# Optimization experiments

Measured on AMD Instinct MI355X. Metric: run time of the kernel, lower is better.

The kernel has to match this reference:

```python
import jax, jax.numpy as jnp
import numpy as np

NUM_CLUSTERS = 16
HIDDEN = 1024
BOTTLENECK = 128
N_TOKENS = 65536


def setup_inputs() -> dict:
    key = jax.random.key(0)
    k_h, k_ids, k_w1, k_b1, k_w2, k_b2 = jax.random.split(key, 6)
    h = jax.random.normal(k_h, (N_TOKENS, HIDDEN), dtype=jnp.float32)
    cluster_ids = jax.random.randint(k_ids, (N_TOKENS,), 0, NUM_CLUSTERS)
    # Stacked per-cluster adapter params (torch Linear: y = x @ W.T + b; we store
    # already-transposed weights so forward is x @ W1[c]).
    s1 = 1.0 / np.sqrt(HIDDEN)
    s2 = 1.0 / np.sqrt(BOTTLENECK)
    W1 = jax.random.uniform(k_w1, (NUM_CLUSTERS, HIDDEN, BOTTLENECK), jnp.float32, -s1, s1)
    b1 = jax.random.uniform(k_b1, (NUM_CLUSTERS, BOTTLENECK), jnp.float32, -s1, s1)
    # Original inits these to zero; use small random values so grads are non-trivial.
    W2 = jax.random.uniform(k_w2, (NUM_CLUSTERS, BOTTLENECK, HIDDEN), jnp.float32, -s2, s2) * 0.02
    b2 = jax.random.uniform(k_b2, (NUM_CLUSTERS, HIDDEN), jnp.float32, -s2, s2) * 0.02
    return {"h": h, "cluster_ids": cluster_ids, "W1": W1, "b1": b1, "W2": W2, "b2": b2}


def reference(h, cluster_ids, W1, b1, W2, b2):
    # h: [N, H]; cluster_ids: [N]; W1: [K, H, B]; b1: [K, B]; W2: [K, B, H]; b2: [K, H]
    # out[n] = h[n] + adapter_{cluster_ids[n]}(h[n])
    K = W1.shape[0]
    out = jnp.zeros_like(h)
    for c in range(K):  # fixed small expert count; select per-token result via where
        mid = jax.nn.gelu(h @ W1[c] + b1[c], approximate=False)  # [N, B]
        y = h + mid @ W2[c] + b2[c]                               # [N, H]
        out = jnp.where((cluster_ids == c)[:, None], y, out)
    return out
```

## Files before the change

### kernel.cpp

```cpp
#include <hip/hip_runtime.h>
#include <hip/hip_bf16.h>
#include <math.h>

#define NUM_CLUSTERS 16
#define HIDDEN 1024
#define BOT 128
#define NTOK 65536

typedef __attribute__((ext_vector_type(8))) short bf16x8;
typedef __attribute__((ext_vector_type(4))) float f32x4;

typedef __attribute__((address_space(3))) unsigned int lds_u32;
typedef const __attribute__((address_space(1))) unsigned int glb_u32;

__device__ __forceinline__ void gload16(const void* g, void* l) {
  __builtin_amdgcn_global_load_lds((glb_u32*)g, (lds_u32*)l, 16, 0, 0);
}

__device__ __forceinline__ unsigned short f2bf(float x) {
  union { float f; unsigned u; } v; v.f = x;
  unsigned r = v.u + 0x7fffu + ((v.u >> 16) & 1u);
  return (unsigned short)(r >> 16);
}

__device__ __forceinline__ bf16x8 pack8(float4 a, float4 b) {
  bf16x8 r;
  r[0] = (short)f2bf(a.x); r[1] = (short)f2bf(a.y);
  r[2] = (short)f2bf(a.z); r[3] = (short)f2bf(a.w);
  r[4] = (short)f2bf(b.x); r[5] = (short)f2bf(b.y);
  r[6] = (short)f2bf(b.z); r[7] = (short)f2bf(b.w);
  return r;
}

#define SWZS(row, sidx) ((sidx) ^ (((row) & 7) << 3))
#define SW4(row, fidx) ((fidx) ^ (((row) & 7) << 2))

#define SCB() __builtin_amdgcn_sched_barrier(0)
#define VMW(n)                                          \
  do {                                                  \
    SCB();                                              \
    asm volatile("s_waitcnt vmcnt(" #n ")" ::: "memory"); \
    SCB();                                              \
  } while (0)
#define SBAR()                                  \
  do {                                          \
    SCB();                                      \
    __builtin_amdgcn_s_barrier();               \
    SCB();                                      \
  } while (0)
#define LGKM0() asm volatile("s_waitcnt lgkmcnt(0)" ::: "memory")

__device__ __forceinline__ int xcd_swz(int bid, int nwg) {
  const int nx = 8;
  int q = nwg / nx, r = nwg % nx;
  int xcd = bid % nx, idx = bid / nx;
  int b = (xcd < r) ? xcd * (q + 1) : r * (q + 1) + (xcd - r) * q;
  return b + idx;
}


__global__ void k_zero(int* p) {
  if (threadIdx.x < 64) p[threadIdx.x] = 0;
}

__global__ void k_hist(const int* __restrict__ ids, int* __restrict__ counts) {
  __shared__ int lh[NUM_CLUSTERS];
  if (threadIdx.x < NUM_CLUSTERS) lh[threadIdx.x] = 0;
  __syncthreads();
  int i = blockIdx.x * blockDim.x + threadIdx.x;
  int stride = gridDim.x * blockDim.x;
  for (; i < NTOK; i += stride) atomicAdd(&lh[ids[i]], 1);
  __syncthreads();
  if (threadIdx.x < NUM_CLUSTERS) atomicAdd(&counts[threadIdx.x], lh[threadIdx.x]);
}

__global__ void k_scan(const int* __restrict__ counts, int* __restrict__ offsets,
                       int* __restrict__ cursor) {
  if (threadIdx.x == 0 && blockIdx.x == 0) {
    int s = 0;
    for (int c = 0; c < NUM_CLUSTERS; ++c) {
      offsets[c] = s; cursor[c] = s; s += counts[c];
    }
    offsets[NUM_CLUSTERS] = s;
  }
}

__global__ void k_scatter(const int* __restrict__ ids, int* cursor,
                          int* __restrict__ perm) {
  __shared__ int lh[NUM_CLUSTERS], lbase[NUM_CLUSTERS];
  const int tid = threadIdx.x;
  if (tid < NUM_CLUSTERS) lh[tid] = 0;
  __syncthreads();
  const int i = blockIdx.x * 256 + tid;
  const int cc = ids[i];
  const int r = atomicAdd(&lh[cc], 1);
  __syncthreads();
  if (tid < NUM_CLUSTERS) lbase[tid] = atomicAdd(&cursor[tid], lh[tid]);
  __syncthreads();
  perm[lbase[cc] + r] = i;
}

__global__ void k_w1til(const float* __restrict__ W1, unsigned short* __restrict__ outw) {
  const int id = blockIdx.x * 256 + threadIdx.x;
  const int c  = id >> 14;
  const int ks = (id >> 10) & 15;
  const int q  = id & 1023;
  const int o  = q << 4;
  const int row = o >> 7;
  const int lb  = (o & 127) ^ ((row & 7) << 4);
  const int k0  = ks * 64 + (lb >> 1);
  const float* src = W1 + ((size_t)c * HIDDEN + k0) * BOT + row;
  unsigned short v[8];
  #pragma unroll
  for (int j = 0; j < 8; ++j) v[j] = f2bf(src[(size_t)j * BOT]);
  *(uint4*)((char*)outw + ((size_t)(c * 16 + ks)) * 16384 + o) = *(const uint4*)v;
}

__global__ void k_w2til(const float* __restrict__ W2, unsigned short* __restrict__ outw) {
  const int id = blockIdx.x * 256 + threadIdx.x;
  const int c  = id >> 14;
  const int nc = (id >> 10) & 15;
  const int q  = id & 1023;
  const int o  = q << 4;
  const int row = o >> 8;
  const int lb  = (o & 255) ^ ((row & 7) << 4);
  const int b0  = lb >> 1;
  const int n   = nc * 64 + row;
  const float* src = W2 + ((size_t)c * BOT + b0) * HIDDEN + n;
  unsigned short v[8];
  #pragma unroll
  for (int j = 0; j < 8; ++j) v[j] = f2bf(src[(size_t)j * HIDDEN]);
  *(uint4*)((char*)outw + ((size_t)(c * 16 + nc)) * 16384 + o) = *(const uint4*)v;
}

__device__ __forceinline__ bool locate(const int* offsets, int bid, int TMv,
                                       int& c, int& base, int& nvalid) {
  int t = bid;
  for (c = 0; c < NUM_CLUSTERS; ++c) {
    int cnt = offsets[c + 1] - offsets[c];
    int nt = (cnt + TMv - 1) / TMv;
    if (t < nt) {
      base = offsets[c] + t * TMv;
      nvalid = min(TMv, offsets[c + 1] - base);
      return true;
    }
    t -= nt;
  }
  return false;
}


__global__ __launch_bounds__(512, 6) void k_gemm1(
    const float* __restrict__ h, const float* __restrict__ b1g,
    const unsigned short* __restrict__ W1til, const int* __restrict__ offsets,
    const int* __restrict__ perm, unsigned short* __restrict__ midg) {

  __shared__ __align__(16) unsigned short sA[2][4096];
  __shared__ __align__(16) unsigned short sB[2][8192];
  __shared__ int sTok[64];

  const int tid = threadIdx.x;
  const int l = tid & 63, w = tid >> 6;
  const int lr = l & 15, lg = l >> 4;
  const int wr = w >> 2, wc = w & 3;
  const int row = tid >> 3, o8 = tid & 7;

  const int nwg = NTOK / 64 + NUM_CLUSTERS;
  int c, base, nvalid;
  if (!locate(offsets, xcd_swz(blockIdx.x, nwg), 64, c, base, nvalid)) return;

  if (tid < 64) sTok[tid] = perm[base + min(tid, nvalid - 1)];
  LGKM0();
  SBAR();

  const unsigned short* w1base = W1til + (size_t)c * 16 * 8192;
  const float* hrow = h + (long)sTok[row] * HIDDEN + o8 * 8;

  float4 vaA[2], vaB[2];
  vaA[0] = *(const float4*)(hrow);       vaA[1] = *(const float4*)(hrow + 4);
  SCB();
  gload16(w1base + tid * 8, &sB[0][tid * 8]);
  gload16(w1base + 4096 + tid * 8, &sB[0][4096 + tid * 8]);
  SCB();
  vaB[0] = *(const float4*)(hrow + 64);  vaB[1] = *(const float4*)(hrow + 68);
  SCB();
  *(bf16x8*)&sA[0][SWZS(row, row * 64 + o8 * 8)] = pack8(vaA[0], vaA[1]);
  LGKM0();
  VMW(2);
  SBAR();

  f32x4 acc[2][2];
  #pragma unroll
  for (int i = 0; i < 2; ++i)
    #pragma unroll
    for (int j = 0; j < 2; ++j) { f32x4 z = {0.f, 0.f, 0.f, 0.f}; acc[i][j] = z; }

#define G1_MFMA(CUR)                                                          \
  do {                                                                        \
    _Pragma("unroll")                                                         \
    for (int kk = 0; kk < 2; ++kk) {                                          \
      bf16x8 af[2], bfr[2];                                                   \
      _Pragma("unroll")                                                       \
      for (int mf = 0; mf < 2; ++mf) {                                        \
        const int m = wr * 32 + mf * 16 + lr;                                 \
        af[mf] = *(const bf16x8*)&sA[CUR][SWZS(m, m * 64 + kk * 32 + lg * 8)];\
      }                                                                       \
      _Pragma("unroll")                                                       \
      for (int nf = 0; nf < 2; ++nf) {                                        \
        const int rn = wc * 32 + nf * 16 + lr;                                \
        bfr[nf] = *(const bf16x8*)&sB[CUR][SWZS(rn, rn * 64 + kk * 32 + lg * 8)]; \
      }                                                                       \
      _Pragma("unroll")                                                       \
      for (int mf = 0; mf < 2; ++mf)                                          \
        _Pragma("unroll")                                                     \
        for (int nf = 0; nf < 2; ++nf)                                        \
          acc[mf][nf] = __builtin_amdgcn_mfma_f32_16x16x32_bf16(              \
              af[mf], bfr[nf], acc[mf][nf], 0, 0, 0);                         \
    }                                                                         \
  } while (0)

  #pragma unroll
  for (int t = 0; t < 16; ++t) {
    const int cur = t & 1;
    if (t < 15) {
      const unsigned short* w1s = w1base + (t + 1) * 8192;
      gload16(w1s + tid * 8, &sB[cur ^ 1][tid * 8]);
      gload16(w1s + 4096 + tid * 8, &sB[cur ^ 1][4096 + tid * 8]);
      SCB();
    }
    if (t < 14) {
      if (t & 1) {
        vaB[0] = *(const float4*)(hrow + (t + 2) * 64);
        vaB[1] = *(const float4*)(hrow + (t + 2) * 64 + 4);
      } else {
        vaA[0] = *(const float4*)(hrow + (t + 2) * 64);
        vaA[1] = *(const float4*)(hrow + (t + 2) * 64 + 4);
      }
      SCB();
    }
    G1_MFMA(cur);
    if (t < 15) {
      const float4* src = ((t + 1) & 1) ? vaB : vaA;
      *(bf16x8*)&sA[cur ^ 1][SWZS(row, row * 64 + o8 * 8)] = pack8(src[0], src[1]);
      if (t < 14) { VMW(2); } else { VMW(0); }
      LGKM0();
      SBAR();
    }
  }
#undef G1_MFMA

  float b1v[2];
  #pragma unroll
  for (int nf = 0; nf < 2; ++nf) b1v[nf] = b1g[c * BOT + wc * 32 + nf * 16 + lr];
  #pragma unroll
  for (int mf = 0; mf < 2; ++mf) {
    #pragma unroll
    for (int nf = 0; nf < 2; ++nf) {
      #pragma unroll
      for (int r = 0; r < 4; ++r) {
        float x = acc[mf][nf][r] + b1v[nf];
        float g = 0.5f * x * (1.0f + erff(x * 0.70710678118654752f));
        const int m = wr * 32 + mf * 16 + lg * 4 + r;
        if (m < nvalid) {
          const int n = wc * 32 + nf * 16 + lr;
          midg[(size_t)(base + m) * BOT + n] = f2bf(g);
        }
      }
    }
  }
}


__global__ __launch_bounds__(512, 6) void k_gemm2(
    const float* __restrict__ h, const float* __restrict__ b2g,
    const unsigned short* __restrict__ W2til, const int* __restrict__ offsets,
    const int* __restrict__ perm, const unsigned short* __restrict__ midg,
    float* __restrict__ out) {

  __shared__ __align__(16) unsigned short sM[8192];
  __shared__ __align__(16) unsigned short sB[2][8192];
  __shared__ int sTok[64];

  const int tid = threadIdx.x;
  const int l = tid & 63, w = tid >> 6;
  const int lr = l & 15, lg = l >> 4;
  const int wr = w >> 2, wc = w & 3;
  const int erow = tid >> 3, eo = tid & 7;

  const int nwg = NTOK / 64 + NUM_CLUSTERS;
  int c, base, nvalid;
  if (!locate(offsets, xcd_swz(blockIdx.x, nwg), 64, c, base, nvalid)) return;

  if (tid < 64) sTok[tid] = perm[base + min(tid, nvalid - 1)];

  const unsigned short* w2base = W2til + (size_t)c * 16 * 8192;

  {
    const int srow = base + min(erow, nvalid - 1);
    const uint4* ms = (const uint4*)(midg + (size_t)srow * BOT + eo * 16);
    uint4 m0 = ms[0], m1 = ms[1];
    SCB();
    gload16(w2base + tid * 8, &sB[0][tid * 8]);
    gload16(w2base + 4096 + tid * 8, &sB[0][4096 + tid * 8]);
    SCB();
    *(uint4*)&sM[SWZS(erow, erow * 128 + eo * 16)]     = m0;
    *(uint4*)&sM[SWZS(erow, erow * 128 + eo * 16 + 8)] = m1;
  }
  LGKM0();
  VMW(0);
  SBAR();

  const long etok = (long)sTok[erow] * HIDDEN;
  const float* hrow = h + etok;
  float* orow = out + etok;
  const bool evalid = erow < nvalid;

  for (int nc = 0; nc < 16; ++nc) {
    const int cur = nc & 1;
    float4 hv0 = *(const float4*)(hrow + nc * 64 + eo * 8);
    float4 hv1 = *(const float4*)(hrow + nc * 64 + eo * 8 + 4);
    float4 bv0 = *(const float4*)(b2g + c * HIDDEN + nc * 64 + eo * 8);
    float4 bv1 = *(const float4*)(b2g + c * HIDDEN + nc * 64 + eo * 8 + 4);
    SCB();
    if (nc < 15) {
      const unsigned short* w2s = w2base + (nc + 1) * 8192;
      gload16(w2s + tid * 8, &sB[cur ^ 1][tid * 8]);
      gload16(w2s + 4096 + tid * 8, &sB[cur ^ 1][4096 + tid * 8]);
      SCB();
    }

    f32x4 acc[2];
    { f32x4 z = {0.f, 0.f, 0.f, 0.f}; acc[0] = z; acc[1] = z; }
    #pragma unroll
    for (int kk = 0; kk < 4; ++kk) {
      bf16x8 af[2], bf1;
      #pragma unroll
      for (int mf = 0; mf < 2; ++mf) {
        const int m = wr * 32 + mf * 16 + lr;
        af[mf] = *(const bf16x8*)&sM[SWZS(m, m * 128 + kk * 32 + lg * 8)];
      }
      const int rn = wc * 16 + lr;
      bf1 = *(const bf16x8*)&sB[cur][SWZS(rn, rn * 128 + kk * 32 + lg * 8)];
      #pragma unroll
      for (int mf = 0; mf < 2; ++mf)
        acc[mf] = __builtin_amdgcn_mfma_f32_16x16x32_bf16(af[mf], bf1, acc[mf], 0, 0, 0);
    }
    SBAR();

    float* sOutF = (float*)&sB[cur][0];
    #pragma unroll
    for (int mf = 0; mf < 2; ++mf) {
      #pragma unroll
      for (int r = 0; r < 4; ++r) {
        const int m = wr * 32 + mf * 16 + lg * 4 + r;
        const int n = wc * 16 + lr;
        sOutF[SW4(m, m * 64 + n)] = acc[mf][r];
      }
    }
    LGKM0();
    SBAR();

    if (evalid) {
      const int fb = erow * 64 + eo * 8;
      const float4 y0 = *(const float4*)&sOutF[SW4(erow, fb)];
      const float4 y1 = *(const float4*)&sOutF[SW4(erow, fb + 4)];
      float4 o0, o1;
      o0.x = y0.x + hv0.x + bv0.x; o0.y = y0.y + hv0.y + bv0.y;
      o0.z = y0.z + hv0.z + bv0.z; o0.w = y0.w + hv0.w + bv0.w;
      o1.x = y1.x + hv1.x + bv1.x; o1.y = y1.y + hv1.y + bv1.y;
      o1.z = y1.z + hv1.z + bv1.z; o1.w = y1.w + hv1.w + bv1.w;
      *(float4*)(orow + nc * 64 + eo * 8)     = o0;
      *(float4*)(orow + nc * 64 + eo * 8 + 4) = o1;
    }
    if (nc < 15) {
      VMW(2);
      SBAR();
    }
  }
}

#define FSWZ(row, sidx) ((sidx) ^ (((row) & 7) << 3))

__global__ __launch_bounds__(256, 2) void k_fused(
    const float* __restrict__ h, const float* __restrict__ b1g,
    const float* __restrict__ b2g, const unsigned short* __restrict__ W1til,
    const unsigned short* __restrict__ W2til, const int* __restrict__ offsets,
    const int* __restrict__ perm, float* __restrict__ out) {

  __shared__ __align__(16) unsigned short sAB[16384];
  __shared__ __align__(16) unsigned short sMid[16384];
  __shared__ int sTok[128];

  const int tid = threadIdx.x;
  const int l = tid & 63, w = tid >> 6;
  const int wr = w >> 1, wc = w & 1;
  const int lr = l & 15, lg = l >> 4;

  int c, base, nvalid;
  if (!locate(offsets, blockIdx.x, 128, c, base, nvalid)) return;

  if (tid < 128) sTok[tid] = perm[base + min(tid, nvalid - 1)];
  __syncthreads();

  const unsigned short* w1base = W1til + (size_t)c * 16 * 8192;
  const unsigned short* w2base = W2til + (size_t)c * 16 * 8192;

  const int arow = tid >> 1, ahalf = tid & 1;
  const long htok = (long)sTok[arow] * HIDDEN;

  f32x4 acc[4][4];
  #pragma unroll
  for (int i = 0; i < 4; ++i)
    #pragma unroll
    for (int j = 0; j < 4; ++j) { f32x4 z = {0.f, 0.f, 0.f, 0.f}; acc[i][j] = z; }

  for (int ks = 0; ks < 16; ++ks) {
    __syncthreads();
    const unsigned short* w1s = w1base + ks * 8192;
    #pragma unroll
    for (int j = 0; j < 4; ++j)
      gload16(w1s + j * 2048 + tid * 8, &sAB[8192 + j * 2048 + tid * 8]);
    {
      const float* hp = h + htok + ks * 64 + ahalf * 32;
      float4 v0 = *(const float4*)(hp + 0),  v1 = *(const float4*)(hp + 4);
      float4 v2 = *(const float4*)(hp + 8),  v3 = *(const float4*)(hp + 12);
      float4 v4 = *(const float4*)(hp + 16), v5 = *(const float4*)(hp + 20);
      float4 v6 = *(const float4*)(hp + 24), v7 = *(const float4*)(hp + 28);
      const int sb = arow * 64 + ahalf * 32;
      *(bf16x8*)&sAB[FSWZ(arow, sb + 0)]  = pack8(v0, v1);
      *(bf16x8*)&sAB[FSWZ(arow, sb + 8)]  = pack8(v2, v3);
      *(bf16x8*)&sAB[FSWZ(arow, sb + 16)] = pack8(v4, v5);
      *(bf16x8*)&sAB[FSWZ(arow, sb + 24)] = pack8(v6, v7);
    }
    __syncthreads();
    #pragma unroll
    for (int kk = 0; kk < 2; ++kk) {
      bf16x8 af[4], bfr[4];
      #pragma unroll
      for (int mf = 0; mf < 4; ++mf) {
        const int rw = wr * 64 + mf * 16 + lr;
        af[mf] = *(const bf16x8*)&sAB[FSWZ(rw, rw * 64 + kk * 32 + lg * 8)];
      }
      #pragma unroll
      for (int nf = 0; nf < 4; ++nf) {
        const int rn = wc * 64 + nf * 16 + lr;
        bfr[nf] = *(const bf16x8*)&sAB[8192 + FSWZ(rn, rn * 64 + kk * 32 + lg * 8)];
      }
      #pragma unroll
      for (int mf = 0; mf < 4; ++mf)
        #pragma unroll
        for (int nf = 0; nf < 4; ++nf)
          acc[mf][nf] = __builtin_amdgcn_mfma_f32_16x16x32_bf16(af[mf], bfr[nf], acc[mf][nf], 0, 0, 0);
    }
  }

  float b1v[4];
  #pragma unroll
  for (int nf = 0; nf < 4; ++nf) b1v[nf] = b1g[c * BOT + wc * 64 + nf * 16 + lr];
  #pragma unroll
  for (int mf = 0; mf < 4; ++mf)
    #pragma unroll
    for (int nf = 0; nf < 4; ++nf)
      #pragma unroll
      for (int r = 0; r < 4; ++r) {
        float x = acc[mf][nf][r] + b1v[nf];
        float g = 0.5f * x * (1.0f + erff(x * 0.70710678118654752f));
        const int m = wr * 64 + mf * 16 + lg * 4 + r;
        const int n = wc * 64 + nf * 16 + lr;
        sMid[FSWZ(m, m * 128 + n)] = f2bf(g);
      }

  for (int nc = 0; nc < 16; ++nc) {
    __syncthreads();
    #pragma unroll
    for (int j = 0; j < 4; ++j)
      gload16(w2base + nc * 8192 + j * 2048 + tid * 8, &sAB[j * 2048 + tid * 8]);
    __syncthreads();

    f32x4 a2[4][2];
    #pragma unroll
    for (int i = 0; i < 4; ++i)
      #pragma unroll
      for (int j = 0; j < 2; ++j) { f32x4 z = {0.f, 0.f, 0.f, 0.f}; a2[i][j] = z; }

    #pragma unroll
    for (int kk = 0; kk < 4; ++kk) {
      bf16x8 af[4], bfr[2];
      #pragma unroll
      for (int mf = 0; mf < 4; ++mf) {
        const int m = wr * 64 + mf * 16 + lr;
        af[mf] = *(const bf16x8*)&sMid[FSWZ(m, m * 128 + kk * 32 + lg * 8)];
      }
      #pragma unroll
      for (int nf = 0; nf < 2; ++nf) {
        const int rn = wc * 32 + nf * 16 + lr;
        bfr[nf] = *(const bf16x8*)&sAB[FSWZ(rn, rn * 128 + kk * 32 + lg * 8)];
      }
      #pragma unroll
      for (int mf = 0; mf < 4; ++mf)
        #pragma unroll
        for (int nf = 0; nf < 2; ++nf)
          a2[mf][nf] = __builtin_amdgcn_mfma_f32_16x16x32_bf16(af[mf], bfr[nf], a2[mf][nf], 0, 0, 0);
    }

    #pragma unroll
    for (int nf = 0; nf < 2; ++nf) {
      const int nn = nc * 64 + wc * 32 + nf * 16 + lr;
      const float b2v = b2g[c * HIDDEN + nn];
      #pragma unroll
      for (int mf = 0; mf < 4; ++mf)
        #pragma unroll
        for (int r = 0; r < 4; ++r) {
          const int m = wr * 64 + mf * 16 + lg * 4 + r;
          if (m < nvalid) {
            const long tk = (long)sTok[m] * HIDDEN;
            out[tk + nn] = h[tk + nn] + a2[mf][nf][r] + b2v;
          }
        }
    }
  }
}

extern "C" void kernel_launch(void* const* d_in, const int* in_sizes, int n_in,
                              void* d_out, int out_size, void* d_ws, size_t ws_size,
                              hipStream_t stream) {
  const float* h   = (const float*)d_in[0];
  const int*   ids = (const int*)d_in[1];
  const float* W1  = (const float*)d_in[2];
  const float* b1  = (const float*)d_in[3];
  const float* W2  = (const float*)d_in[4];
  const float* b2  = (const float*)d_in[5];
  float* out = (float*)d_out;

  char* ws = (char*)d_ws;
  int* counts  = (int*)ws;
  int* cursor  = (int*)(ws + 64);
  int* offsets = (int*)(ws + 128);
  int* perm    = (int*)(ws + 256);
  unsigned short* W1til = (unsigned short*)(ws + 262400);
  unsigned short* W2til = W1til + (size_t)16 * 16 * 8192;
  unsigned short* midg  = W2til + (size_t)16 * 16 * 8192;
  const size_t need = 262400 + 2 * (size_t)16 * 16 * 8192 * 2 +
                      (size_t)NTOK * BOT * 2;

  k_zero<<<1, 64, 0, stream>>>(counts);
  k_hist<<<256, 256, 0, stream>>>(ids, counts);
  k_scan<<<1, 64, 0, stream>>>(counts, offsets, cursor);
  k_scatter<<<NTOK / 256, 256, 0, stream>>>(ids, cursor, perm);
  k_w1til<<<1024, 256, 0, stream>>>(W1, W1til);
  k_w2til<<<1024, 256, 0, stream>>>(W2, W2til);

  if (ws_size >= need) {
    const int nwg = NTOK / 64 + NUM_CLUSTERS;
    k_gemm1<<<nwg, 512, 0, stream>>>(h, b1, W1til, offsets, perm, midg);
    k_gemm2<<<nwg, 512, 0, stream>>>(h, b2, W2til, offsets, perm, midg, out);
  } else {
    k_fused<<<NTOK / 128 + NUM_CLUSTERS, 256, 0, stream>>>(
        h, b1, b2, W1til, W2til, offsets, perm, out);
  }
}
```

Before: 270.3 us.

## Rewrite gemm2 to read fragment-ordered W2 directly from global, dropping LDS staging

Adds a k_w2lin prepack that stores W2 in MFMA B-fragment order, so each lane loads its operand with one contiguous 16-byte global read. k_gemm2 drops to 256 threads: each wave owns 16 token rows and keeps its mid A-fragments in registers, and all W2 staging through LDS is removed along with the block-wide barriers. LDS is now used only for a per-wave epilogue transpose. The cost is that every wave rereads W2 tiles from global/L2 instead of sharing them through LDS, and the per-wave work per block is larger.

Result: slower. 330.4 us (+22.2%).

```diff
diff --git a/kernel.cpp b/kernel.cpp
--- a/kernel.cpp
+++ b/kernel.cpp
@@ -116,6 +116,22 @@
   *(uint4*)((char*)outw + ((size_t)(c * 16 + ks)) * 16384 + o) = *(const uint4*)v;
 }
 
+__global__ void k_w2lin(const float* __restrict__ W2, unsigned short* __restrict__ outw) {
+  const int id = blockIdx.x * 256 + threadIdx.x;
+  const int c   = id >> 14;
+  const int rem = id & 16383;
+  const int fg  = rem >> 6;
+  const int l   = rem & 63;
+  const int nc  = fg >> 4, kk = (fg >> 2) & 3, nf = fg & 3;
+  const int n   = nc * 64 + nf * 16 + (l & 15);
+  const int k0  = kk * 32 + (l >> 4) * 8;
+  const float* src = W2 + ((size_t)c * BOT + k0) * HIDDEN + n;
+  unsigned short v[8];
+  #pragma unroll
+  for (int j = 0; j < 8; ++j) v[j] = f2bf(src[(size_t)j * HIDDEN]);
+  *(uint4*)(outw + (size_t)id * 8) = *(const uint4*)v;
+}
+
 __global__ void k_w2til(const float* __restrict__ W2, unsigned short* __restrict__ outw) {
   const int id = blockIdx.x * 256 + threadIdx.x;
   const int c  = id >> 14;
@@ -148,7 +164,6 @@
   }
   return false;
 }
-
 
 __global__ __launch_bounds__(512, 6) void k_gemm1(
     const float* __restrict__ h, const float* __restrict__ b1g,
@@ -271,110 +286,87 @@
 }
 
 
-__global__ __launch_bounds__(512, 6) void k_gemm2(
+__global__ __launch_bounds__(256, 5) void k_gemm2(
     const float* __restrict__ h, const float* __restrict__ b2g,
-    const unsigned short* __restrict__ W2til, const int* __restrict__ offsets,
+    const unsigned short* __restrict__ W2lin, const int* __restrict__ offsets,
     const int* __restrict__ perm, const unsigned short* __restrict__ midg,
     float* __restrict__ out) {
 
-  __shared__ __align__(16) unsigned short sM[8192];
-  __shared__ __align__(16) unsigned short sB[2][8192];
+  __shared__ __align__(16) float sOut[4 * 1024];
   __shared__ int sTok[64];
 
   const int tid = threadIdx.x;
   const int l = tid & 63, w = tid >> 6;
   const int lr = l & 15, lg = l >> 4;
-  const int wr = w >> 2, wc = w & 3;
-  const int erow = tid >> 3, eo = tid & 7;
 
   const int nwg = NTOK / 64 + NUM_CLUSTERS;
   int c, base, nvalid;
   if (!locate(offsets, xcd_swz(blockIdx.x, nwg), 64, c, base, nvalid)) return;
 
   if (tid < 64) sTok[tid] = perm[base + min(tid, nvalid - 1)];
-
-  const unsigned short* w2base = W2til + (size_t)c * 16 * 8192;
-
-  {
-    const int srow = base + min(erow, nvalid - 1);
-    const uint4* ms = (const uint4*)(midg + (size_t)srow * BOT + eo * 16);
-    uint4 m0 = ms[0], m1 = ms[1];
-    SCB();
-    gload16(w2base + tid * 8, &sB[0][tid * 8]);
-    gload16(w2base + 4096 + tid * 8, &sB[0][4096 + tid * 8]);
-    SCB();
-    *(uint4*)&sM[SWZS(erow, erow * 128 + eo * 16)]     = m0;
-    *(uint4*)&sM[SWZS(erow, erow * 128 + eo * 16 + 8)] = m1;
-  }
-  LGKM0();
-  VMW(0);
-  SBAR();
-
+  __syncthreads();
+
+  const long amrow = (long)(base + min(w * 16 + lr, nvalid - 1)) * BOT;
+  bf16x8 ma[4];
+  #pragma unroll
+  for (int kk = 0; kk < 4; ++kk)
+    ma[kk] = *(const bf16x8*)(midg + amrow + kk * 32 + lg * 8);
+
+  const unsigned short* wlin = W2lin + (size_t)c * 131072;
+
+  const int er = l >> 2, ecg = l & 3;
+  const int erow = w * 16 + er;
+  const bool evalid = erow < nvalid;
   const long etok = (long)sTok[erow] * HIDDEN;
   const float* hrow = h + etok;
   float* orow = out + etok;
-  const bool evalid = erow < nvalid;
+  float* sW = sOut + w * 1024;
+  const float* b2c = b2g + c * HIDDEN;
 
   for (int nc = 0; nc < 16; ++nc) {
-    const int cur = nc & 1;
-    float4 hv0 = *(const float4*)(hrow + nc * 64 + eo * 8);
-    float4 hv1 = *(const float4*)(hrow + nc * 64 + eo * 8 + 4);
-    float4 bv0 = *(const float4*)(b2g + c * HIDDEN + nc * 64 + eo * 8);
-    float4 bv1 = *(const float4*)(b2g + c * HIDDEN + nc * 64 + eo * 8 + 4);
-    SCB();
-    if (nc < 15) {
-      const unsigned short* w2s = w2base + (nc + 1) * 8192;
-      gload16(w2s + tid * 8, &sB[cur ^ 1][tid * 8]);
-      gload16(w2s + 4096 + tid * 8, &sB[cur ^ 1][4096 + tid * 8]);
-      SCB();
-    }
-
-    f32x4 acc[2];
-    { f32x4 z = {0.f, 0.f, 0.f, 0.f}; acc[0] = z; acc[1] = z; }
+    const unsigned short* fbp = wlin + nc * 8192;
+
+    f32x4 acc[4];
+    #pragma unroll
+    for (int i = 0; i < 4; ++i) { f32x4 z = {0.f, 0.f, 0.f, 0.f}; acc[i] = z; }
+
     #pragma unroll
     for (int kk = 0; kk < 4; ++kk) {
-      bf16x8 af[2], bf1;
-      #pragma unroll
-      for (int mf = 0; mf < 2; ++mf) {
-        const int m = wr * 32 + mf * 16 + lr;
-        af[mf] = *(const bf16x8*)&sM[SWZS(m, m * 128 + kk * 32 + lg * 8)];
-      }
-      const int rn = wc * 16 + lr;
-      bf1 = *(const bf16x8*)&sB[cur][SWZS(rn, rn * 128 + kk * 32 + lg * 8)];
-      #pragma unroll
-      for (int mf = 0; mf < 2; ++mf)
-        acc[mf] = __builtin_amdgcn_mfma_f32_16x16x32_bf16(af[mf], bf1, acc[mf], 0, 0, 0);
-    }
-    SBAR();
-
-    float* sOutF = (float*)&sB[cur][0];
-    #pragma unroll
-    for (int mf = 0; mf < 2; ++mf) {
+      #pragma unroll
+      for (int nf = 0; nf < 4; ++nf) {
+        const bf16x8 bf = *(const bf16x8*)(fbp + (kk * 4 + nf) * 512 + l * 8);
+        acc[nf] = __builtin_amdgcn_mfma_f32_16x16x32_bf16(ma[kk], bf, acc[nf], 0, 0, 0);
+      }
+    }
+
+    float4 hv[4], bv[4];
+    #pragma unroll
+    for (int j = 0; j < 4; ++j) {
+      hv[j] = *(const float4*)(hrow + nc * 64 + ecg * 16 + j * 4);
+      bv[j] = *(const float4*)(b2c + nc * 64 + ecg * 16 + j * 4);
+    }
+
+    #pragma unroll
+    for (int nf = 0; nf < 4; ++nf) {
       #pragma unroll
       for (int r = 0; r < 4; ++r) {
-        const int m = wr * 32 + mf * 16 + lg * 4 + r;
-        const int n = wc * 16 + lr;
-        sOutF[SW4(m, m * 64 + n)] = acc[mf][r];
-      }
-    }
-    LGKM0();
-    SBAR();
-
+        const int m = lg * 4 + r;
+        const int n = nf * 16 + lr;
+        sW[SW4(m, m * 64 + n)] = acc[nf][r];
+      }
+    }
     if (evalid) {
-      const int fb = erow * 64 + eo * 8;
-      const float4 y0 = *(const float4*)&sOutF[SW4(erow, fb)];
-      const float4 y1 = *(const float4*)&sOutF[SW4(erow, fb + 4)];
-      float4 o0, o1;
-      o0.x = y0.x + hv0.x + bv0.x; o0.y = y0.y + hv0.y + bv0.y;
-      o0.z = y0.z + hv0.z + bv0.z; o0.w = y0.w + hv0.w + bv0.w;
-      o1.x = y1.x + hv1.x + bv1.x; o1.y = y1.y + hv1.y + bv1.y;
-      o1.z = y1.z + hv1.z + bv1.z; o1.w = y1.w + hv1.w + bv1.w;
-      *(float4*)(orow + nc * 64 + eo * 8)     = o0;
-      *(float4*)(orow + nc * 64 + eo * 8 + 4) = o1;
-    }
-    if (nc < 15) {
-      VMW(2);
-      SBAR();
+      #pragma unroll
+      for (int j = 0; j < 4; ++j) {
+        const int fo = er * 64 + ecg * 16 + j * 4;
+        const float4 y = *(const float4*)&sW[SW4(er, fo)];
+        float4 o;
+        o.x = y.x + hv[j].x + bv[j].x;
+        o.y = y.y + hv[j].y + bv[j].y;
+        o.z = y.z + hv[j].z + bv[j].z;
+        o.w = y.w + hv[j].w + bv[j].w;
+        *(float4*)(orow + nc * 64 + ecg * 16 + j * 4) = o;
+      }
     }
   }
 }
@@ -538,8 +530,8 @@
   int* offsets = (int*)(ws + 128);
   int* perm    = (int*)(ws + 256);
   unsigned short* W1til = (unsigned short*)(ws + 262400);
-  unsigned short* W2til = W1til + (size_t)16 * 16 * 8192;
-  unsigned short* midg  = W2til + (size_t)16 * 16 * 8192;
+  unsigned short* W2buf = W1til + (size_t)16 * 16 * 8192;
+  unsigned short* midg  = W2buf + (size_t)16 * 16 * 8192;
   const size_t need = 262400 + 2 * (size_t)16 * 16 * 8192 * 2 +
                       (size_t)NTOK * BOT * 2;
 
@@ -548,14 +540,15 @@
   k_scan<<<1, 64, 0, stream>>>(counts, offsets, cursor);
   k_scatter<<<NTOK / 256, 256, 0, stream>>>(ids, cursor, perm);
   k_w1til<<<1024, 256, 0, stream>>>(W1, W1til);
-  k_w2til<<<1024, 256, 0, stream>>>(W2, W2til);
 
   if (ws_size >= need) {
+    k_w2lin<<<1024, 256, 0, stream>>>(W2, W2buf);
     const int nwg = NTOK / 64 + NUM_CLUSTERS;
     k_gemm1<<<nwg, 512, 0, stream>>>(h, b1, W1til, offsets, perm, midg);
-    k_gemm2<<<nwg, 512, 0, stream>>>(h, b2, W2til, offsets, perm, midg, out);
+    k_gemm2<<<nwg, 256, 0, stream>>>(h, b2, W2buf, offsets, perm, midg, out);
   } else {
+    k_w2til<<<1024, 256, 0, stream>>>(W2, W2buf);
     k_fused<<<NTOK / 128 + NUM_CLUSTERS, 256, 0, stream>>>(
-        h, b1, b2, W1til, W2til, offsets, perm, out);
-  }
-}
+        h, b1, b2, W1til, W2buf, offsets, perm, out);
+  }
+}
```
